# Kernel optimization log

Measured on AMD Instinct MI355X. Metric: run time of the kernel, lower is better.

The kernel has to match this reference:

```python
import jax, jax.numpy as jnp
import numpy as np

B, Q, DIN, DOUT = 1, 1024, 4096, 4096
H, G, HD = 32, 8, 128          # heads, kv groups, head_dim; group_size = H // G
PREV = 3072                     # cached KV length
MAXPOS = 4096                   # rope table length (>= PREV + Q)
START = PREV


def _rope_tables(max_pos, head_dim):
    half = head_dim // 2
    inv_freq = 1.0 / (10000.0 ** (jnp.arange(half, dtype=jnp.float32) / half))
    ang = jnp.arange(max_pos, dtype=jnp.float32)[:, None] * inv_freq[None, :]
    ang = jnp.concatenate([ang, ang], axis=-1)  # [max_pos, head_dim]
    return jnp.cos(ang), jnp.sin(ang)


def apply_rope(x, cos, sin, start_pos):
    # x: [b, h, s, d]; rotate-half RoPE with absolute positions start_pos..start_pos+s
    s, d = x.shape[2], x.shape[3]
    c = cos[start_pos:start_pos + s]  # [s, d] (start_pos is a Python int)
    sn = sin[start_pos:start_pos + s]
    x1, x2 = x[..., : d // 2], x[..., d // 2:]
    rotated = jnp.concatenate([-x2, x1], axis=-1)
    return x * c + rotated * sn


def setup_inputs() -> dict:
    key = jax.random.key(0)
    ks = jax.random.split(key, 7)
    x = jax.random.normal(ks[0], (B, Q, DIN), dtype=jnp.float32)
    cos, sin = _rope_tables(MAXPOS, HD)
    # causal mask: query at abs position START+i may attend kv position j <= START+i
    qpos = START + jnp.arange(Q)
    kpos = jnp.arange(START + Q)
    mask = (kpos[None, :] > qpos[:, None])[None, None]  # [1,1,Q,KV], True = masked
    prev_k = jax.random.normal(ks[1], (B, G, PREV, HD), dtype=jnp.float32)
    prev_v = jax.random.normal(ks[2], (B, G, PREV, HD), dtype=jnp.float32)
    sc = 0.02
    Wq = jax.random.normal(ks[3], (DIN, DOUT), dtype=jnp.float32) * sc
    Wk = jax.random.normal(ks[4], (DIN, G * HD), dtype=jnp.float32) * sc
    Wv = jax.random.normal(ks[5], (DIN, G * HD), dtype=jnp.float32) * sc
    Wo = jax.random.normal(ks[6], (DOUT, DOUT), dtype=jnp.float32) * sc
    return dict(x=x, mask=mask, cos=cos, sin=sin, start_pos=START,
                prev_k=prev_k, prev_v=prev_v, Wq=Wq, Wk=Wk, Wv=Wv, Wo=Wo)


def reference(x, mask, cos, sin, start_pos, prev_k, prev_v, Wq, Wk, Wv, Wo):
    b, s, _ = x.shape
    gs = H // G  # group_size
    q = (x @ Wq).reshape(b, s, H, HD).transpose(0, 2, 1, 3)   # [b,H,s,hd]
    k = (x @ Wk).reshape(b, s, G, HD).transpose(0, 2, 1, 3)   # [b,G,s,hd]
    v = (x @ Wv).reshape(b, s, G, HD).transpose(0, 2, 1, 3)
    q = apply_rope(q, cos, sin, start_pos)
    k = apply_rope(k, cos, sin, start_pos)
    keys = jnp.concatenate([prev_k, k], axis=2)    # [b,G,KV,hd]
    values = jnp.concatenate([prev_v, v], axis=2)
    # grouped attention (equivalent to repeat_interleave of K/V over group_size)
    qg = q.reshape(b, G, gs, s, HD)
    scores = jnp.einsum('bgnqd,bgkd->bgnqk', qg, keys)        # [b,G,gs,s,KV]
    scores = jnp.where(mask[:, :, None], -jnp.inf, scores)
    attn = jax.nn.softmax(scores / np.sqrt(HD).astype(np.float32), axis=-1)
    ctx = jnp.einsum('bgnqk,bgkd->bgnqd', attn, values)       # [b,G,gs,s,hd]
    ctx = ctx.reshape(b, H, s, HD).transpose(0, 2, 1, 3).reshape(b, s, DOUT)
    out = ctx @ Wo
    return (out, keys, values)
```

## Files before the change

### kernel.cpp

```cpp
#include <hip/hip_runtime.h>

typedef unsigned short u16;
typedef unsigned int u32;
typedef __attribute__((ext_vector_type(4))) float f32x4;
typedef __attribute__((ext_vector_type(16))) float f32x16;
typedef __attribute__((ext_vector_type(8))) __bf16 bf16x8;
typedef __attribute__((ext_vector_type(4))) u16 u16x4;
typedef __attribute__((ext_vector_type(8))) u16 u16x8;
typedef __attribute__((ext_vector_type(4))) u32 u32x4;

#define START_POS 3072
#define NKV 4096
#define HD_ 128
#define SEQ 1024
#define DIN_ 4096
#define DQKV 6144

__device__ __forceinline__ void gll16(const void* g, void* l) {
  __builtin_amdgcn_global_load_lds((const __attribute__((address_space(1))) u32*)g,
                                   (__attribute__((address_space(3))) u32*)l, 16, 0, 0);
}
__device__ __forceinline__ u16 f2bf(float f) {
  u32 u = __builtin_bit_cast(u32, f);
  return (u16)((u + 0x7fffu + ((u >> 16) & 1u)) >> 16);
}
__device__ __forceinline__ u32 pack2bf(float a, float b) {
  return (u32)f2bf(a) | ((u32)f2bf(b) << 16);
}
__device__ __forceinline__ f32x4 mfma16(bf16x8 a, bf16x8 b, f32x4 c) {
  return __builtin_amdgcn_mfma_f32_16x16x32_bf16(a, b, c, 0, 0, 0);
}
__device__ __forceinline__ f32x16 mfma32(bf16x8 a, bf16x8 b, f32x16 c) {
  return __builtin_amdgcn_mfma_f32_32x32x16_bf16(a, b, c, 0, 0, 0);
}

__global__ __launch_bounds__(256) void wtrans(const float* __restrict__ W,
    u16* __restrict__ Wt, int N, int ntn, int row_off)
{
  __shared__ float T[64][68];
  int bid = blockIdx.x;
  int nt = bid % ntn, kt = bid / ntn;
  int t = threadIdx.x;
  int kl = t >> 4, nl4 = (t & 15) << 2;
#pragma unroll
  for (int r = 0; r < 4; r++) {
    int row = r * 16 + kl;
    f32x4 v = *(const f32x4*)(W + (size_t)(kt * 64 + row) * N + nt * 64 + nl4);
    T[row][nl4] = v[0]; T[row][nl4 + 1] = v[1]; T[row][nl4 + 2] = v[2]; T[row][nl4 + 3] = v[3];
  }
  __syncthreads();
  int nl = t >> 2, k0 = (t & 3) << 4;
  u16x8 lo, hi;
#pragma unroll
  for (int j = 0; j < 8; j++) lo[j] = f2bf(T[k0 + j][nl]);
#pragma unroll
  for (int j = 0; j < 8; j++) hi[j] = f2bf(T[k0 + 8 + j][nl]);
  u16* dst = Wt + (size_t)(row_off + nt * 64 + nl) * 4096 + kt * 64 + k0;
  *(u16x8*)dst = lo;
  *(u16x8*)(dst + 8) = hi;
}

__global__ __launch_bounds__(256) void cvt_bf16(const float* __restrict__ src,
    u16* __restrict__ dst, int n4)
{
  int i = blockIdx.x * 256 + threadIdx.x;
  if (i >= n4) return;
  f32x4 v = *(const f32x4*)(src + (size_t)i * 4);
  u16x4 o;
#pragma unroll
  for (int j = 0; j < 4; j++) o[j] = f2bf(v[j]);
  *(u16x4*)(dst + (size_t)i * 4) = o;
}

__global__ __launch_bounds__(256) void gemm_bt(
    const u16* __restrict__ A, const u16* __restrict__ Bt,
    float* __restrict__ C, int N, int K, int nbx)
{
  __shared__ u16 As[128 * 32];
  __shared__ u16 Bs[64 * 32];
  int nwg = (int)gridDim.x;
  int orig = blockIdx.x;
  int q8 = nwg >> 3, r8 = nwg & 7;
  int xcd = orig & 7, jj = orig >> 3;
  int wgid = (xcd < r8 ? xcd * (q8 + 1) : r8 * (q8 + 1) + (xcd - r8) * q8) + jj;
  int by = wgid / nbx, bx = wgid % nbx;
  int tid = threadIdx.x, lane = tid & 63, wid = tid >> 6;
  int wr = wid >> 1, wc = wid & 1;
  int c = lane & 15, hh = lane >> 4;
  int lrow = wid * 16 + (lane >> 2);
  int ksl = (lane & 3) << 3;
  const u16* aS0 = A + (size_t)(by * 128 + lrow) * K + ksl;
  const u16* bS0 = Bt + (size_t)(bx * 64 + lrow) * K + ksl;
  u16* aL0 = As + wid * 512;
  u16* bL0 = Bs + wid * 512;
  f32x4 acc[4][2] = {};
  for (int k0 = 0; k0 < K; k0 += 32) {
    gll16(aS0 + k0, aL0);
    gll16(aS0 + (size_t)64 * K + k0, aL0 + 2048);
    gll16(bS0 + k0, bL0);
    __syncthreads();
    bf16x8 af[4], bf[2];
#pragma unroll
    for (int i = 0; i < 4; i++)
      af[i] = *(const bf16x8*)(As + (wr * 64 + i * 16 + c) * 32 + hh * 8);
#pragma unroll
    for (int i = 0; i < 2; i++)
      bf[i] = *(const bf16x8*)(Bs + (wc * 32 + i * 16 + c) * 32 + hh * 8);
#pragma unroll
    for (int mi = 0; mi < 4; mi++)
#pragma unroll
      for (int ni = 0; ni < 2; ni++)
        acc[mi][ni] = mfma16(af[mi], bf[ni], acc[mi][ni]);
    __syncthreads();
  }
  int row0 = by * 128 + wr * 64 + hh * 4;
  int col0 = bx * 64 + wc * 32 + c;
#pragma unroll
  for (int mi = 0; mi < 4; mi++)
#pragma unroll
    for (int ni = 0; ni < 2; ni++)
#pragma unroll
      for (int i = 0; i < 4; i++)
        C[(size_t)(row0 + mi * 16 + i) * N + col0 + ni * 16] = acc[mi][ni][i];
}

__global__ __launch_bounds__(256) void rope_q(const float* __restrict__ qkv,
    const float* __restrict__ cosb, const float* __restrict__ sinb, u16* __restrict__ qb)
{
  int tid = blockIdx.x * 256 + threadIdx.x;
  int dq = tid & 15, h = (tid >> 4) & 31, s = tid >> 9;
  int d = dq << 2;
  const float* base = qkv + (size_t)s * DQKV + h * HD_ + d;
  f32x4 a = *(const f32x4*)base;
  f32x4 b2 = *(const f32x4*)(base + 64);
  f32x4 cc = *(const f32x4*)(cosb + (size_t)(START_POS + s) * HD_ + d);
  f32x4 sn = *(const f32x4*)(sinb + (size_t)(START_POS + s) * HD_ + d);
  u16x4 o1, o2;
#pragma unroll
  for (int i = 0; i < 4; i++) {
    o1[i] = f2bf(a[i] * cc[i] - b2[i] * sn[i]);
    o2[i] = f2bf(b2[i] * cc[i] + a[i] * sn[i]);
  }
  u16* dst = qb + ((size_t)h * SEQ + s) * HD_ + d;
  *(u16x4*)dst = o1;
  *(u16x4*)(dst + 64) = o2;
}

__global__ __launch_bounds__(256) void rope_k(const float* __restrict__ qkv,
    const float* __restrict__ cosb, const float* __restrict__ sinb,
    float* __restrict__ keys, u16* __restrict__ kbb)
{
  int tid = blockIdx.x * 256 + threadIdx.x;
  int dq = tid & 15, g = (tid >> 4) & 7, s = tid >> 7;
  int d = dq << 2;
  const float* base = qkv + (size_t)s * DQKV + DIN_ + g * HD_ + d;
  f32x4 a = *(const f32x4*)base;
  f32x4 b2 = *(const f32x4*)(base + 64);
  f32x4 cc = *(const f32x4*)(cosb + (size_t)(START_POS + s) * HD_ + d);
  f32x4 sn = *(const f32x4*)(sinb + (size_t)(START_POS + s) * HD_ + d);
  f32x4 o1, o2;
  u16x4 p1, p2;
#pragma unroll
  for (int i = 0; i < 4; i++) {
    o1[i] = a[i] * cc[i] - b2[i] * sn[i];
    o2[i] = b2[i] * cc[i] + a[i] * sn[i];
    p1[i] = f2bf(o1[i]);
    p2[i] = f2bf(o2[i]);
  }
  size_t off = ((size_t)g * NKV + START_POS + s) * HD_ + d;
  *(f32x4*)(keys + off) = o1;
  *(f32x4*)(keys + off + 64) = o2;
  *(u16x4*)(kbb + off) = p1;
  *(u16x4*)(kbb + off + 64) = p2;
}

__global__ __launch_bounds__(256) void copy_vnew(const float* __restrict__ qkv,
    float* __restrict__ values)
{
  int tid = blockIdx.x * 256 + threadIdx.x;
  int dq = tid & 31, g = (tid >> 5) & 7, s = tid >> 8;
  int d = dq << 2;
  f32x4 v = *(const f32x4*)(qkv + (size_t)s * DQKV + DIN_ + 1024 + g * HD_ + d);
  *(f32x4*)(values + ((size_t)g * NKV + START_POS + s) * HD_ + d) = v;
}

__global__ __launch_bounds__(256) void prev_copy(const float* __restrict__ pk,
    const float* __restrict__ pv, float* __restrict__ keys, float* __restrict__ values,
    u16* __restrict__ kbb)
{
  int idx = blockIdx.x * 256 + threadIdx.x;
  int d4 = idx & 31;
  int rest = idx >> 5;
  int p = rest % 3072, g = rest / 3072;
  f32x4 kq = *(const f32x4*)(pk + (size_t)idx * 4);
  f32x4 vq = *(const f32x4*)(pv + (size_t)idx * 4);
  size_t off = ((size_t)g * NKV + p) * HD_ + d4 * 4;
  *(f32x4*)(keys + off) = kq;
  *(f32x4*)(values + off) = vq;
  u16x4 kb4;
#pragma unroll
  for (int i = 0; i < 4; i++) kb4[i] = f2bf(kq[i]);
  *(u16x4*)(kbb + off) = kb4;
}

__global__ __launch_bounds__(256) void vtrans(const float* __restrict__ pv,
    const float* __restrict__ qkv, u16* __restrict__ vT)
{
  __shared__ float T[64][68];
  int bid = blockIdx.x;
  int dt = bid & 1, pt = (bid >> 1) & 63, g = bid >> 7;
  int t = threadIdx.x;
  int pl = t >> 4, dl4 = (t & 15) << 2;
#pragma unroll
  for (int r = 0; r < 4; r++) {
    int row = r * 16 + pl;
    int pos = pt * 64 + row;
    f32x4 v;
    if (pos < START_POS)
      v = *(const f32x4*)(pv + ((size_t)g * START_POS + pos) * HD_ + dt * 64 + dl4);
    else
      v = *(const f32x4*)(qkv + (size_t)(pos - START_POS) * DQKV + 5120 + g * HD_ + dt * 64 + dl4);
    T[row][dl4] = v[0]; T[row][dl4 + 1] = v[1]; T[row][dl4 + 2] = v[2]; T[row][dl4 + 3] = v[3];
  }
  __syncthreads();
  int dl = t >> 2, p0 = (t & 3) << 4;
  u16x8 lo, hi;
#pragma unroll
  for (int j = 0; j < 8; j++) lo[j] = f2bf(T[p0 + j][dl]);
#pragma unroll
  for (int j = 0; j < 8; j++) hi[j] = f2bf(T[p0 + 8 + j][dl]);
  u16* dst = vT + ((size_t)g * HD_ + dt * 64 + dl) * NKV + pt * 64 + p0;
  *(u16x8*)dst = lo;
  *(u16x8*)(dst + 8) = hi;
}

__global__ __launch_bounds__(128, 2) void attn_fwd(
    const u16* __restrict__ qb, const u16* __restrict__ kb,
    const u16* __restrict__ vT, float* __restrict__ Opart, float* __restrict__ Ml)
{
  __shared__ u16 Ks[2 * 32 * 128];
  __shared__ u16 Vs[2 * 128 * 32];
  const float C2 = 0.12751744f;
  int bid = blockIdx.x;
  int g = bid & 7, j = bid >> 3;
  int sp = j >> 6, jj = j & 63;
  int h = g * 4 + (jj >> 4), qt = jj & 15;
  int tid = threadIdx.x, lane = tid & 63, w = tid >> 6;
  int c32 = lane & 31, h8 = lane >> 5;
  int qw0 = qt * 64 + w * 32;
  bf16x8 Qf[8];
#pragma unroll
  for (int dc = 0; dc < 8; dc++)
    Qf[dc] = *(const bf16x8*)(qb + ((size_t)(h * 1024 + qw0 + c32)) * 128 + dc * 16 + h8 * 8);
  f32x16 O0 = {}, O1 = {}, O2 = {}, O3 = {};
  float Mx = -1e30f, Ls = 0.f;
  int t0 = sp ? (49 + qt) : 0;
  int t1 = sp ? (98 + 2 * qt) : (49 + qt);

#define STAGE_KV(tt, bo) do { \
  _Pragma("unroll") \
  for (int r = 0; r < 4; r++) { \
    int s = w * 256 + r * 64 + lane; \
    int krow = s >> 4, sl = s & 15; \
    gll16(kb + ((size_t)(g * 4096 + (tt) * 32 + krow)) * 128 + (sl ^ (krow & 7)) * 8, \
          Ks + (bo) + (w * 256 + r * 64) * 8); \
    int d = s >> 2, sl2 = s & 3; \
    gll16(vT + ((size_t)(g * 128 + d)) * 4096 + (tt) * 32 + (sl2 ^ ((d >> 1) & 3)) * 8, \
          Vs + (bo) + (w * 256 + r * 64) * 8); \
  } \
} while (0)

  int cur = 0;
  STAGE_KV(t0, 0);
  __syncthreads();
  int vxr = (c32 >> 1) & 3;
  for (int t = t0; t < t1; t++) {
    if (t + 1 < t1) STAGE_KV(t + 1, (cur ^ 1) * 4096);
    const u16* Kb = Ks + cur * 4096;
    const u16* Vb = Vs + cur * 4096;
    f32x16 S0 = {};
#pragma unroll
    for (int dc = 0; dc < 8; dc++) {
      int sx = (2 * dc + h8) ^ (c32 & 7);
      bf16x8 k0 = *(const bf16x8*)(Kb + (size_t)c32 * 128 + sx * 8);
      S0 = mfma32(k0, Qf[dc], S0);
    }
    if (t * 32 + 31 > START_POS + qw0) {
      int qa = START_POS + qw0 + c32;
#pragma unroll
      for (int r = 0; r < 16; r++) {
        int kvo = t * 32 + (r & 3) + 8 * (r >> 2) + 4 * h8;
        if (kvo > qa) S0[r] = -1e30f;
      }
    }
    float tm[16];
#pragma unroll
    for (int r = 0; r < 16; r++) tm[r] = S0[r];
#pragma unroll
    for (int sft = 8; sft >= 1; sft >>= 1)
#pragma unroll
      for (int r = 0; r < sft; r++) tm[r] = fmaxf(tm[r], tm[r + sft]);
    float full = fmaxf(tm[0], __shfl_xor(tm[0], 32));
    if (!__all(full <= Mx + 62.0f)) {
      float Mn = fmaxf(Mx, full);
      float al = exp2f((Mx - Mn) * C2);
      Mx = Mn;
      Ls *= al;
#pragma unroll
      for (int r = 0; r < 16; r++) { O0[r] *= al; O1[r] *= al; O2[r] *= al; O3[r] *= al; }
    }
#pragma unroll
    for (int r = 0; r < 16; r++) S0[r] = exp2f((S0[r] - Mx) * C2);
    float ts[16];
#pragma unroll
    for (int r = 0; r < 16; r++) ts[r] = S0[r];
#pragma unroll
    for (int sft = 8; sft >= 1; sft >>= 1)
#pragma unroll
      for (int r = 0; r < sft; r++) ts[r] = ts[r] + ts[r + sft];
    Ls += ts[0] + __shfl_xor(ts[0], 32);
    u32 pk0[8], x0[8];
#pragma unroll
    for (int m = 0; m < 8; m++) pk0[m] = pack2bf(S0[2 * m], S0[2 * m + 1]);
#pragma unroll
    for (int m = 0; m < 8; m++) x0[m] = __shfl_xor(pk0[m], 32);
    bf16x8 pbf[2];
    {
      u32x4 f0 = { h8 ? x0[2] : pk0[0], h8 ? x0[3] : pk0[1],
                   h8 ? pk0[2] : x0[0], h8 ? pk0[3] : x0[1] };
      u32x4 f1 = { h8 ? x0[6] : pk0[4], h8 ? x0[7] : pk0[5],
                   h8 ? pk0[6] : x0[4], h8 ? pk0[7] : x0[5] };
      pbf[0] = __builtin_bit_cast(bf16x8, f0);
      pbf[1] = __builtin_bit_cast(bf16x8, f1);
    }
#pragma unroll
    for (int kc = 0; kc < 2; kc++) {
      int sv = 2 * kc + h8;
      int sx = (sv ^ vxr) * 8;
      {
        bf16x8 vf = *(const bf16x8*)(Vb + (size_t)(0 * 32 + c32) * 32 + sx);
        O0 = mfma32(vf, pbf[kc], O0);
      }
      {
        bf16x8 vf = *(const bf16x8*)(Vb + (size_t)(1 * 32 + c32) * 32 + sx);
        O1 = mfma32(vf, pbf[kc], O1);
      }
      {
        bf16x8 vf = *(const bf16x8*)(Vb + (size_t)(2 * 32 + c32) * 32 + sx);
        O2 = mfma32(vf, pbf[kc], O2);
      }
      {
        bf16x8 vf = *(const bf16x8*)(Vb + (size_t)(3 * 32 + c32) * 32 + sx);
        O3 = mfma32(vf, pbf[kc], O3);
      }
    }
    __syncthreads();
    cur ^= 1;
  }
#undef STAGE_KV
  {
    float* Orow = Opart + (size_t)sp * 4194304 + (size_t)(qw0 + c32) * 4096 + h * 128;
#pragma unroll
    for (int a = 0; a < 4; a++) {
      f32x4 o0, o1, o2, o3;
#pragma unroll
      for (int b = 0; b < 4; b++) {
        o0[b] = O0[4 * a + b]; o1[b] = O1[4 * a + b];
        o2[b] = O2[4 * a + b]; o3[b] = O3[4 * a + b];
      }
      int d0 = 8 * a + 4 * h8;
      *(f32x4*)(Orow + d0) = o0;
      *(f32x4*)(Orow + 32 + d0) = o1;
      *(f32x4*)(Orow + 64 + d0) = o2;
      *(f32x4*)(Orow + 96 + d0) = o3;
    }
    if (h8 == 0) {
      float* mp = Ml + ((size_t)(sp * 32 + h) * 1024 + qw0 + c32) * 2;
      mp[0] = Mx; mp[1] = Ls;
    }
  }
}

__global__ __launch_bounds__(256) void attn_combine(const float* __restrict__ Opart,
    const float* __restrict__ Ml, u16* __restrict__ ctxb)
{
  int idx = blockIdx.x * 256 + threadIdx.x;
  int q = idx >> 10, c4 = idx & 1023;
  int col = c4 * 4, h = col >> 7;
  const float* m0p = Ml + ((size_t)h * 1024 + q) * 2;
  const float* m1p = Ml + ((size_t)(32 + h) * 1024 + q) * 2;
  float m0 = m0p[0], l0 = m0p[1];
  float m1 = m1p[0], l1 = m1p[1];
  float M = fmaxf(m0, m1);
  float w0 = exp2f((m0 - M) * 0.12751744f);
  float w1 = exp2f((m1 - M) * 0.12751744f);
  float inv = 1.0f / (l0 * w0 + l1 * w1);
  f32x4 a = *(const f32x4*)(Opart + (size_t)q * 4096 + col);
  f32x4 b = *(const f32x4*)(Opart + 4194304 + (size_t)q * 4096 + col);
  u16x4 o;
#pragma unroll
  for (int i = 0; i < 4; i++) o[i] = f2bf((a[i] * w0 + b[i] * w1) * inv);
  *(u16x4*)(ctxb + (size_t)q * 4096 + col) = o;
}

extern "C" void kernel_launch(void* const* d_in, const int* in_sizes, int n_in,
                              void* d_out, int out_size, void* d_ws, size_t ws_size,
                              hipStream_t stream) {
  const float* x      = (const float*)d_in[0];
  const float* cosb   = (const float*)d_in[2];
  const float* sinb   = (const float*)d_in[3];
  const float* prev_k = (const float*)d_in[5];
  const float* prev_v = (const float*)d_in[6];
  const float* Wq     = (const float*)d_in[7];
  const float* Wk     = (const float*)d_in[8];
  const float* Wv     = (const float*)d_in[9];
  const float* Wo     = (const float*)d_in[10];

  u16* Wt_proj = (u16*)d_ws;
  u16* Wt_out  = Wt_proj + (size_t)6144 * 4096;
  u16* xb      = Wt_out + (size_t)4096 * 4096;
  float* qkv   = (float*)(xb + (size_t)1024 * 4096);
  u16* qb      = (u16*)(qkv + (size_t)1024 * 6144);
  u16* kbb     = qb + (size_t)32 * 1024 * 128;
  u16* vT      = kbb + (size_t)8 * 4096 * 128;
  u16* ctxb    = vT + (size_t)8 * 4096 * 128;
  float* Opart = (float*)d_ws;
  float* Ml    = Opart + (size_t)2 * 1024 * 4096;

  float* outp   = (float*)d_out;
  float* keys   = outp + (size_t)4194304;
  float* values = outp + (size_t)8388608;

  wtrans<<<4096, 256, 0, stream>>>(Wq, Wt_proj, 4096, 64, 0);
  wtrans<<<1024, 256, 0, stream>>>(Wk, Wt_proj, 1024, 16, 4096);
  wtrans<<<1024, 256, 0, stream>>>(Wv, Wt_proj, 1024, 16, 5120);
  wtrans<<<4096, 256, 0, stream>>>(Wo, Wt_out, 4096, 64, 0);
  cvt_bf16<<<4096, 256, 0, stream>>>(x, xb, 1048576);

  gemm_bt<<<768, 256, 0, stream>>>(xb, Wt_proj, qkv, 6144, 4096, 96);

  rope_q<<<2048, 256, 0, stream>>>(qkv, cosb, sinb, qb);
  rope_k<<<512, 256, 0, stream>>>(qkv, cosb, sinb, keys, kbb);
  copy_vnew<<<1024, 256, 0, stream>>>(qkv, values);
  prev_copy<<<3072, 256, 0, stream>>>(prev_k, prev_v, keys, values, kbb);
  vtrans<<<1024, 256, 0, stream>>>(prev_v, qkv, vT);

  attn_fwd<<<1024, 128, 0, stream>>>(qb, kbb, vT, Opart, Ml);
  attn_combine<<<4096, 256, 0, stream>>>(Opart, Ml, ctxb);

  gemm_bt<<<512, 256, 0, stream>>>(ctxb, Wt_out, outp, 4096, 4096, 64);
}
```

Baseline: 401.9 us.

## Double-buffer GEMM LDS tiles, split QK accumulators, add setprio, use hip bf16 pack

The bf16 GEMM now keeps two LDS buffers and issues the next K-tile's global-to-LDS loads before computing the current one, so memory latency overlaps MFMA work and one barrier per iteration is dropped. In the attention kernel the QK^T MFMA chain is split across two accumulators to shorten the dependency chain. s_setprio brackets are placed around the MFMA blocks in both kernels. The bf16 packing helper now uses the HIP __float22bfloat162_rn intrinsic. The GEMM's LDS footprint doubles, which may reduce occupancy, and the split accumulator costs extra registers plus a final add.

```diff
diff --git a/kernel.cpp b/kernel.cpp
--- a/kernel.cpp
+++ b/kernel.cpp
@@ -1,4 +1,5 @@
 #include <hip/hip_runtime.h>
+#include <hip/hip_bf16.h>
 
 typedef unsigned short u16;
 typedef unsigned int u32;
@@ -25,7 +26,9 @@
   return (u16)((u + 0x7fffu + ((u >> 16) & 1u)) >> 16);
 }
 __device__ __forceinline__ u32 pack2bf(float a, float b) {
-  return (u32)f2bf(a) | ((u32)f2bf(b) << 16);
+  __hip_bfloat162 t = __float22bfloat162_rn(float2{a, b});
+  u32 u; __builtin_memcpy(&u, &t, 4);
+  return u;
 }
 __device__ __forceinline__ f32x4 mfma16(bf16x8 a, bf16x8 b, f32x4 c) {
   return __builtin_amdgcn_mfma_f32_16x16x32_bf16(a, b, c, 0, 0, 0);
@@ -76,8 +79,8 @@
     const u16* __restrict__ A, const u16* __restrict__ Bt,
     float* __restrict__ C, int N, int K, int nbx)
 {
-  __shared__ u16 As[128 * 32];
-  __shared__ u16 Bs[64 * 32];
+  __shared__ u16 As[2 * 128 * 32];
+  __shared__ u16 Bs[2 * 64 * 32];
   int nwg = (int)gridDim.x;
   int orig = blockIdx.x;
   int q8 = nwg >> 3, r8 = nwg & 7;
@@ -91,28 +94,40 @@
   int ksl = (lane & 3) << 3;
   const u16* aS0 = A + (size_t)(by * 128 + lrow) * K + ksl;
   const u16* bS0 = Bt + (size_t)(bx * 64 + lrow) * K + ksl;
-  u16* aL0 = As + wid * 512;
-  u16* bL0 = Bs + wid * 512;
+
+#define GSTAGE(buf, kk) do { \
+  gll16(aS0 + (kk), As + (buf) * 4096 + wid * 512); \
+  gll16(aS0 + (size_t)64 * K + (kk), As + (buf) * 4096 + 2048 + wid * 512); \
+  gll16(bS0 + (kk), Bs + (buf) * 2048 + wid * 512); \
+} while (0)
+
   f32x4 acc[4][2] = {};
-  for (int k0 = 0; k0 < K; k0 += 32) {
-    gll16(aS0 + k0, aL0);
-    gll16(aS0 + (size_t)64 * K + k0, aL0 + 2048);
-    gll16(bS0 + k0, bL0);
-    __syncthreads();
+  int nk = K >> 5;
+  int cur = 0;
+  GSTAGE(0, 0);
+  __syncthreads();
+  for (int kt = 0; kt < nk; kt++) {
+    if (kt + 1 < nk) GSTAGE(cur ^ 1, (kt + 1) * 32);
+    const u16* Ab = As + cur * 4096;
+    const u16* Bb = Bs + cur * 2048;
     bf16x8 af[4], bf[2];
 #pragma unroll
     for (int i = 0; i < 4; i++)
-      af[i] = *(const bf16x8*)(As + (wr * 64 + i * 16 + c) * 32 + hh * 8);
+      af[i] = *(const bf16x8*)(Ab + (wr * 64 + i * 16 + c) * 32 + hh * 8);
 #pragma unroll
     for (int i = 0; i < 2; i++)
-      bf[i] = *(const bf16x8*)(Bs + (wc * 32 + i * 16 + c) * 32 + hh * 8);
+      bf[i] = *(const bf16x8*)(Bb + (wc * 32 + i * 16 + c) * 32 + hh * 8);
+    __builtin_amdgcn_s_setprio(1);
 #pragma unroll
     for (int mi = 0; mi < 4; mi++)
 #pragma unroll
       for (int ni = 0; ni < 2; ni++)
         acc[mi][ni] = mfma16(af[mi], bf[ni], acc[mi][ni]);
+    __builtin_amdgcn_s_setprio(0);
     __syncthreads();
-  }
+    cur ^= 1;
+  }
+#undef GSTAGE
   int row0 = by * 128 + wr * 64 + hh * 4;
   int col0 = bx * 64 + wc * 32 + c;
 #pragma unroll
@@ -278,13 +293,20 @@
     if (t + 1 < t1) STAGE_KV(t + 1, (cur ^ 1) * 4096);
     const u16* Kb = Ks + cur * 4096;
     const u16* Vb = Vs + cur * 4096;
-    f32x16 S0 = {};
-#pragma unroll
-    for (int dc = 0; dc < 8; dc++) {
-      int sx = (2 * dc + h8) ^ (c32 & 7);
-      bf16x8 k0 = *(const bf16x8*)(Kb + (size_t)c32 * 128 + sx * 8);
-      S0 = mfma32(k0, Qf[dc], S0);
-    }
+    f32x16 S0 = {}, Sb = {};
+    __builtin_amdgcn_s_setprio(1);
+#pragma unroll
+    for (int dc = 0; dc < 8; dc += 2) {
+      int sxA = (2 * dc + h8) ^ (c32 & 7);
+      int sxB = (2 * dc + 2 + h8) ^ (c32 & 7);
+      bf16x8 kA = *(const bf16x8*)(Kb + (size_t)c32 * 128 + sxA * 8);
+      bf16x8 kB = *(const bf16x8*)(Kb + (size_t)c32 * 128 + sxB * 8);
+      S0 = mfma32(kA, Qf[dc], S0);
+      Sb = mfma32(kB, Qf[dc + 1], Sb);
+    }
+    __builtin_amdgcn_s_setprio(0);
+#pragma unroll
+    for (int r = 0; r < 16; r++) S0[r] += Sb[r];
     if (t * 32 + 31 > START_POS + qw0) {
       int qa = START_POS + qw0 + c32;
 #pragma unroll
@@ -333,6 +355,7 @@
       pbf[0] = __builtin_bit_cast(bf16x8, f0);
       pbf[1] = __builtin_bit_cast(bf16x8, f1);
     }
+    __builtin_amdgcn_s_setprio(1);
 #pragma unroll
     for (int kc = 0; kc < 2; kc++) {
       int sv = 2 * kc + h8;
@@ -354,6 +377,7 @@
         O3 = mfma32(vf, pbf[kc], O3);
       }
     }
+    __builtin_amdgcn_s_setprio(0);
     __syncthreads();
     cur ^= 1;
   }
```

New measurement: 379.2 us. -5.6%, faster.
